# Kernel tuning notes

Hardware: AMD Instinct MI355X
Metric: run time of the kernel (lower is better)

The kernel has to match this reference:

```python
import jax, jax.numpy as jnp
import numpy as np
import math

B, H, N, D = 2, 16, 2048, 128
SM_SCALE = 1.0 / math.sqrt(D)


def setup_inputs() -> dict:
    key = jax.random.key(0)
    kq, kk, kv = jax.random.split(key, 3)
    q = jax.random.normal(kq, (B, H, N, D), dtype=jnp.float32)
    k = jax.random.normal(kk, (B, H, N, D), dtype=jnp.float32)
    v = jax.random.normal(kv, (B, H, N, D), dtype=jnp.float32)
    return {"q": q, "k": k, "v": v}


def reference(q, k, v):
    # RBF-kernel causal attention (non-softmax):
    #   logits_ij = -sm_scale * ||q_i - k_j||^2
    #            = 2*sm_scale*q_i.k_j - sm_scale*||q_i||^2 - sm_scale*||k_j||^2
    #   p = exp(logits) with causal mask (p_ij = 0 for j > i); out = p @ v
    sm_scale = jnp.float32(SM_SCALE)
    q_sq = sm_scale * jnp.sum(q * q, axis=-1)  # [B,H,N]
    k_sq = sm_scale * jnp.sum(k * k, axis=-1)  # [B,H,N]
    qk = jnp.einsum("bhmd,bhnd->bhmn", q, k)
    logits = (2.0 * sm_scale) * qk - q_sq[..., :, None] - k_sq[..., None, :]
    n = q.shape[2]
    causal = jnp.tril(jnp.ones((n, n), dtype=bool))
    logits = jnp.where(causal, logits, -jnp.inf)
    p = jnp.exp(logits)  # NOT normalized (non-softmax attention)
    out = jnp.einsum("bhmn,bhnd->bhmd", p, v)
    return out
```

## Files before the change

kernel.cpp:

```cpp
#include <hip/hip_runtime.h>
#include <math.h>


#define NSEQ 2048
#define DH   128
#define BHC  32
#define SM_SCALE 0.08838834764831845f

typedef __attribute__((ext_vector_type(8))) short    short8;
typedef __attribute__((ext_vector_type(8))) _Float16 half8;
typedef __attribute__((ext_vector_type(4))) short    short4_;
typedef __attribute__((ext_vector_type(4))) float    float4_;
typedef __attribute__((ext_vector_type(4))) unsigned uint4_;
typedef __attribute__((ext_vector_type(2))) unsigned uint2_;

#define KST 136
#define VST 72

__device__ __forceinline__ short f2bf(float x){
  union{float f; unsigned u;} a; a.f=x;
  unsigned r = a.u + 0x7fffu + ((a.u>>16)&1u);
  return (short)(r>>16);
}
__device__ __forceinline__ float bf2f(short h){
  union{float f; unsigned u;} a; a.u=((unsigned)(unsigned short)h)<<16; return a.f;
}
__device__ __forceinline__ unsigned packbf(float a, float b){
  return (unsigned)(unsigned short)f2bf(a) | ((unsigned)(unsigned short)f2bf(b)<<16);
}
__device__ __forceinline__ unsigned cvtpk_bf16(float a, float b){
  unsigned r;
  asm("v_cvt_pk_bf16_f32 %0, %1, %2" : "=v"(r) : "v"(a), "v"(b));
  return r;
}

__device__ __forceinline__ void qswap32(unsigned A, unsigned B, unsigned &X, unsigned &Y){
  uint2_ r = __builtin_amdgcn_permlane32_swap(A, B, false, false);
  X = r[0]; Y = r[1];
}
__device__ __forceinline__ void qswap16(unsigned A, unsigned B, unsigned &X, unsigned &Y, int oddq){
#if __has_builtin(__builtin_amdgcn_permlane16_swap)
  uint2_ r = __builtin_amdgcn_permlane16_swap(A, B, false, false);
  X = r[0]; Y = r[1];
#else
  unsigned As = (unsigned)__builtin_amdgcn_ds_swizzle((int)A, 0x401F);
  unsigned Bs = (unsigned)__builtin_amdgcn_ds_swizzle((int)B, 0x401F);
  X = oddq ? Bs : A;
  Y = oddq ? B  : As;
#endif
}

__global__ __launch_bounds__(256)
void prep_kv5(const float* __restrict__ kg, const float* __restrict__ vg,
              _Float16* __restrict__ khg, short* __restrict__ vtg,
              float* __restrict__ ksqg){
  __shared__ unsigned Vls[128*33];
  const int b = blockIdx.x, t = threadIdx.x;
  const int l = t & 63, wv = t >> 6;
  if(b < 1024){
    const int bh = b>>5, jt = b&31;
    const float4_* vb4 = (const float4_*)(vg + ((size_t)bh*NSEQ + (size_t)jt*64)*DH);
    #pragma unroll
    for(int i=0;i<8;++i){
      float4_ own = vb4[i*256 + t];
      float4_ par;
      par.x = __shfl_xor(own.x, 32); par.y = __shfl_xor(own.y, 32);
      par.z = __shfl_xor(own.z, 32); par.w = __shfl_xor(own.w, 32);
      const int hi = (l>>5)&1;
      unsigned w0 = hi ? packbf(par.z, own.z) : packbf(own.x, par.x);
      unsigned w1 = hi ? packbf(par.w, own.w) : packbf(own.y, par.y);
      const int dd = 4*(t&31) + 2*hi;
      const int j2 = 4*i + wv;
      Vls[dd*33 + j2]     = w0;
      Vls[(dd+1)*33 + j2] = w1;
    }
    __syncthreads();
    short* outp = vtg + ((size_t)(bh*32 + jt)*DH)*64;
    #pragma unroll
    for(int it=0; it<4; ++it){
      int idx = t + 256*it;
      int d = idx>>3, slot = idx&7;
      uint4_ o;
      o.x = Vls[d*33 + 4*slot];   o.y = Vls[d*33 + 4*slot+1];
      o.z = Vls[d*33 + 4*slot+2]; o.w = Vls[d*33 + 4*slot+3];
      *(uint4_*)(outp + d*64 + 8*slot) = o;
    }
  } else {
    const int kb = b - 1024;
    const float4_* kb4 = (const float4_*)(kg + (size_t)kb*64*DH);
    #pragma unroll
    for(int i=0;i<8;++i){
      float4_ x = kb4[i*256 + t];
      const int row = 64*kb + 8*i + (t>>5);
      const int d   = 4*(t&31);
      union{ _Float16 h[4]; uint2_ u; } pk;
      pk.h[0]=(_Float16)x.x; pk.h[1]=(_Float16)x.y;
      pk.h[2]=(_Float16)x.z; pk.h[3]=(_Float16)x.w;
      *(uint2_*)(khg + (size_t)row*DH + d) = pk.u;
      float ss = x.x*x.x + x.y*x.y + x.z*x.z + x.w*x.w;
      ss += __shfl_xor(ss,1);  ss += __shfl_xor(ss,2);
      ss += __shfl_xor(ss,4);  ss += __shfl_xor(ss,8);
      ss += __shfl_xor(ss,16);
      if((l&31)==0) ksqg[row] = SM_SCALE*ss;
    }
  }
}

__global__ __launch_bounds__(256)
void rbf_attn10(const float* __restrict__ qg,
                const _Float16* __restrict__ khg,
                const short* __restrict__ vtg,
                const float* __restrict__ ksqg,
                float* __restrict__ og){
  __shared__ short Kst[2][64*KST];
  __shared__ short Vst[2][128*VST];
  __shared__ float ksLs[2][64];

  const int tid=threadIdx.x;
  const int w=tid>>6, l=tid&63;
  const int quad=l>>4, lr=l&15;
  const int bh=blockIdx.x;
  const int y = blockIdx.y;
  const int t = (y<8) ? y : 23-y;
  const int qbase = 128*t + 32*w;
  const int jtmax = 2*t+1;

  const float*    Qg = qg   + (size_t)bh*NSEQ*DH;
  const _Float16* Kh = khg  + (size_t)bh*NSEQ*DH;
  const short*    Vt = vtg  + (size_t)bh*32*DH*64;
  const float*    Ks = ksqg + (size_t)bh*NSEQ;
  float*          Og = og   + (size_t)bh*NSEQ*DH;

  half8 qf[2][4];
  float qsq[2];
  #pragma unroll
  for(int rt=0;rt<2;++rt){
    const int qrow = qbase + 16*rt + lr;
    const float* qp = Qg + (size_t)qrow*DH + 8*quad;
    float ss=0.f;
    #pragma unroll
    for(int ks=0;ks<4;++ks){
      float4_ a = *(const float4_*)(qp + 32*ks);
      float4_ b = *(const float4_*)(qp + 32*ks + 4);
      half8 h;
      #pragma unroll
      for(int j=0;j<4;++j){
        h[j]   = (_Float16)a[j];
        h[j+4] = (_Float16)b[j];
        ss += a[j]*a[j] + b[j]*b[j];
      }
      qf[rt][ks]=h;
    }
    ss += __shfl_xor(ss,16);
    ss += __shfl_xor(ss,32);
    qsq[rt] = SM_SCALE*ss;
  }

  float4_ oacc[2][8];
  #pragma unroll
  for(int a=0;a<2;++a)
    #pragma unroll
    for(int b2=0;b2<8;++b2) oacc[a][b2] = (float4_)0.f;

  uint4_ kreg[4], vreg[4];
  float  kqreg = 0.f;
  {
    #pragma unroll
    for(int it=0;it<4;++it){
      int idx = tid + 256*it;
      int row = idx>>4, c = idx&15;
      kreg[it] = *(const uint4_*)(Kh + (size_t)row*DH + 8*c);
      int d = idx>>3, slot = idx&7;
      vreg[it] = *(const uint4_*)(Vt + (size_t)d*64 + 8*slot);
    }
    if(tid<64) kqreg = Ks[tid];
  }
  {
    #pragma unroll
    for(int it=0;it<4;++it){
      int idx = tid + 256*it;
      int row = idx>>4, c = idx&15;
      *(uint4_*)&Kst[0][row*KST + 8*c] = kreg[it];
      int d = idx>>3, slot = idx&7;
      *(uint4_*)&Vst[0][d*VST + 8*slot] = vreg[it];
    }
    if(tid<64) ksLs[0][tid] = kqreg;
  }

  int cur = 0;
  for(int jt=0; jt<=jtmax; ++jt){
    __syncthreads();

    if(jt < jtmax){
      const int jc2 = (jt+1)*64;
      #pragma unroll
      for(int it=0;it<4;++it){
        int idx = tid + 256*it;
        int row = idx>>4, c = idx&15;
        kreg[it] = *(const uint4_*)(Kh + (size_t)(jc2+row)*DH + 8*c);
        int d = idx>>3, slot = idx&7;
        vreg[it] = *(const uint4_*)(Vt + ((size_t)(jt+1)*DH + d)*64 + 8*slot);
      }
      if(tid<64) kqreg = Ks[jc2 + tid];
    }

    const int rel = qbase + 31 - 64*jt;
    if(rel >= 0){
      const int ctmax = (rel>>4) < 3 ? (rel>>4) : 3;
      const int nks2  = (rel >= 32) ? 2 : 1;

      float4_ sacc[2][4];
      #pragma unroll
      for(int a=0;a<2;++a)
        #pragma unroll
        for(int ct=0;ct<4;++ct) sacc[a][ct] = (float4_)0.f;

      __builtin_amdgcn_s_setprio(1);
      #pragma unroll
      for(int ks=0;ks<4;++ks){
        half8 kf[4];
        #pragma unroll
        for(int ct=0;ct<4;++ct)
          if(ct<=ctmax) kf[ct] = *(const half8*)&Kst[cur][(16*ct+lr)*KST + 32*ks + 8*quad];
        #pragma unroll
        for(int ct=0;ct<4;++ct)
          if(ct<=ctmax){
            sacc[0][ct]=__builtin_amdgcn_mfma_f32_16x16x32_f16(kf[ct],qf[0][ks],sacc[0][ct],0,0,0);
            sacc[1][ct]=__builtin_amdgcn_mfma_f32_16x16x32_f16(kf[ct],qf[1][ks],sacc[1][ct],0,0,0);
          }
      }
      __builtin_amdgcn_s_setprio(0);

      unsigned pk[2][4][2];
      {
        const int jg0 = 64*jt;
        #pragma unroll
        for(int rt=0;rt<2;++rt){
          const int qrow = qbase + 16*rt + lr;
          const float qs = qsq[rt];
          #pragma unroll
          for(int ct=0;ct<4;++ct){
            if(ct < 2*nks2){
              float4_ kq = *(const float4_*)&ksLs[cur][16*ct + 4*quad];
              const int j0 = jg0 + 16*ct + 4*quad;
              float p[4];
              #pragma unroll
              for(int r=0;r<4;++r){
                float logit = (2.f*SM_SCALE)*sacc[rt][ct][r] - qs - kq[r];
                p[r] = (j0 + r <= qrow) ? __expf(logit) : 0.f;
              }
              pk[rt][ct][0] = cvtpk_bf16(p[0], p[1]);
              pk[rt][ct][1] = cvtpk_bf16(p[2], p[3]);
            }
          }
        }
      }

      __builtin_amdgcn_s_setprio(1);
      #pragma unroll
      for(int ks2=0;ks2<2;++ks2){
        if(ks2 < nks2){
          short8 pf[2];
          #pragma unroll
          for(int rt=0;rt<2;++rt){
            unsigned A0,B0,A1,B1;
            qswap32(pk[rt][2*ks2][0], pk[rt][2*ks2+1][0], A0, B0);
            qswap32(pk[rt][2*ks2][1], pk[rt][2*ks2+1][1], A1, B1);
            unsigned w0,w1,w2,w3;
            qswap16(A0, B0, w0, w2, quad&1);
            qswap16(A1, B1, w1, w3, quad&1);
            union{ uint4_ u; short8 s; } pfu;
            pfu.u.x=w0; pfu.u.y=w1; pfu.u.z=w2; pfu.u.w=w3;
            pf[rt] = pfu.s;
          }
          #pragma unroll
          for(int ctv=0;ctv<8;++ctv){
            const short8 vf = *(const short8*)&Vst[cur][(16*ctv+lr)*VST + 32*ks2 + 8*quad];
            oacc[0][ctv]=__builtin_amdgcn_mfma_f32_16x16x32_bf16(pf[0],vf,oacc[0][ctv],0,0,0);
            oacc[1][ctv]=__builtin_amdgcn_mfma_f32_16x16x32_bf16(pf[1],vf,oacc[1][ctv],0,0,0);
          }
        }
      }
      __builtin_amdgcn_s_setprio(0);
    }

    if(jt < jtmax){
      const int nxt = cur^1;
      #pragma unroll
      for(int it=0;it<4;++it){
        int idx = tid + 256*it;
        int row = idx>>4, c = idx&15;
        *(uint4_*)&Kst[nxt][row*KST + 8*c] = kreg[it];
        int d = idx>>3, slot = idx&7;
        *(uint4_*)&Vst[nxt][d*VST + 8*slot] = vreg[it];
      }
      if(tid<64) ksLs[nxt][tid] = kqreg;
    }
    cur ^= 1;
  }

  #pragma unroll
  for(int rt=0;rt<2;++rt)
    #pragma unroll
    for(int ctv=0;ctv<8;++ctv)
      #pragma unroll
      for(int r=0;r<4;++r){
        const int qrow = qbase + 16*rt + 4*quad + r;
        Og[(size_t)qrow*DH + 16*ctv + lr] = oacc[rt][ctv][r];
      }
}

#define KSTf 136
#define VSTf 36
#define PSTf 72

__global__ __launch_bounds__(256,2)
void rbf_attn_mfma(const float* __restrict__ qg, const float* __restrict__ kg,
                   const float* __restrict__ vg, float* __restrict__ og){
  __shared__ short    Khi[64*KSTf];
  __shared__ short    Klo[64*KSTf];
  __shared__ unsigned VP [128*VSTf];
  __shared__ short    Pfb[64*PSTf];
  __shared__ float    qsq_s[64];
  __shared__ float    ksq_s[64];

  const int tid=threadIdx.x;
  const int w=tid>>6, l=tid&63;
  const int wr=w>>1, wc=w&1;
  const int quad=l>>4, lr=l&15;
  const int bh=blockIdx.x, yp=blockIdx.y;

  const float* Qg = qg + (size_t)bh*NSEQ*DH;
  const float* Kg = kg + (size_t)bh*NSEQ*DH;
  const float* Vg = vg + (size_t)bh*NSEQ*DH;
  float*       Og = og + (size_t)bh*NSEQ*DH;

  for(int pass=0;pass<2;++pass){
    const int m = pass ? (31-yp) : yp;
    __syncthreads();
    short8 qhf[2][4], qlf[2][4];
    #pragma unroll
    for(int rt=0;rt<2;++rt){
      const int grow = m*64 + 32*wr + 16*rt + lr;
      const float* qp = Qg + (size_t)grow*DH + 8*quad;
      float ss=0.f;
      #pragma unroll
      for(int ks=0;ks<4;++ks){
        float4_ a = *(const float4_*)(qp + 32*ks);
        float4_ b = *(const float4_*)(qp + 32*ks + 4);
        short8 hi, lo;
        #pragma unroll
        for(int j=0;j<4;++j){
          float fa=a[j], fb=b[j];
          short ha=f2bf(fa); hi[j]=ha;   lo[j]=f2bf(fa-bf2f(ha));
          short hb=f2bf(fb); hi[j+4]=hb; lo[j+4]=f2bf(fb-bf2f(hb));
          ss += fa*fa + fb*fb;
        }
        qhf[rt][ks]=hi; qlf[rt][ks]=lo;
      }
      ss += __shfl_xor(ss,16);
      ss += __shfl_xor(ss,32);
      if(wc==0 && quad==0) qsq_s[32*wr+16*rt+lr] = SM_SCALE*ss;
    }
    float4_ oacc[2][4];
    #pragma unroll
    for(int a=0;a<2;++a)
      #pragma unroll
      for(int b=0;b<4;++b) oacc[a][b] = (float4_)0.f;

    const int ntiles = m+1;
    for(int jt=0;jt<ntiles;++jt){
      const int jc = jt*64;
      __syncthreads();
      #pragma unroll
      for(int it=0;it<4;++it){
        const int i = tid + 256*it;
        const int row = i>>4, c0 = 8*(i&15);
        const float* kp = Kg + (size_t)(jc+row)*DH + c0;
        float4_ a = *(const float4_*)kp;
        float4_ b = *(const float4_*)(kp+4);
        short8 hi, lo;
        float ss=0.f;
        #pragma unroll
        for(int j=0;j<4;++j){
          float fa=a[j], fb=b[j];
          short ha=f2bf(fa); hi[j]=ha;   lo[j]=f2bf(fa-bf2f(ha));
          short hb=f2bf(fb); hi[j+4]=hb; lo[j+4]=f2bf(fb-bf2f(hb));
          ss += fa*fa + fb*fb;
        }
        ss += __shfl_xor(ss,1); ss += __shfl_xor(ss,2);
        ss += __shfl_xor(ss,4); ss += __shfl_xor(ss,8);
        if(lr==0) ksq_s[row] = SM_SCALE*ss;
        *(short8*)&Khi[row*KSTf + c0] = hi;
        *(short8*)&Klo[row*KSTf + c0] = lo;
      }
      #pragma unroll
      for(int it=0;it<4;++it){
        const int u = tid + 256*it;
        const int d = u & 127, jg = u >> 7;
        const float* vp = Vg + (size_t)(jc + 8*jg)*DH + d;
        float vv[8];
        #pragma unroll
        for(int jj=0;jj<8;++jj) vv[jj] = vp[(size_t)jj*DH];
        uint4_ pk;
        #pragma unroll
        for(int p2=0;p2<4;++p2)
          pk[p2] = (unsigned)(unsigned short)f2bf(vv[2*p2]) |
                   ((unsigned)(unsigned short)f2bf(vv[2*p2+1])<<16);
        *(uint4_*)&VP[d*VSTf + 4*jg] = pk;
      }
      __syncthreads();
      float4_ sacc[2][2];
      #pragma unroll
      for(int a=0;a<2;++a)
        #pragma unroll
        for(int b=0;b<2;++b) sacc[a][b] = (float4_)0.f;
      #pragma unroll
      for(int ks=0;ks<4;++ks){
        short8 khf[2], klf[2];
        #pragma unroll
        for(int ct=0;ct<2;++ct){
          const int off = (32*wc + 16*ct + lr)*KSTf + 32*ks + 8*quad;
          khf[ct] = *(const short8*)&Khi[off];
          klf[ct] = *(const short8*)&Klo[off];
        }
        #pragma unroll
        for(int rt=0;rt<2;++rt)
          #pragma unroll
          for(int ct=0;ct<2;++ct){
            sacc[rt][ct]=__builtin_amdgcn_mfma_f32_16x16x32_bf16(qhf[rt][ks],khf[ct],sacc[rt][ct],0,0,0);
            sacc[rt][ct]=__builtin_amdgcn_mfma_f32_16x16x32_bf16(qhf[rt][ks],klf[ct],sacc[rt][ct],0,0,0);
            sacc[rt][ct]=__builtin_amdgcn_mfma_f32_16x16x32_bf16(qlf[rt][ks],khf[ct],sacc[rt][ct],0,0,0);
          }
      }
      #pragma unroll
      for(int rt=0;rt<2;++rt){
        float qs[4];
        #pragma unroll
        for(int r=0;r<4;++r) qs[r]=qsq_s[32*wr+16*rt+4*quad+r];
        #pragma unroll
        for(int ct=0;ct<2;++ct){
          const float ksq = ksq_s[32*wc+16*ct+lr];
          const int colg = jc + 32*wc+16*ct+lr;
          #pragma unroll
          for(int r=0;r<4;++r){
            const int rowg = m*64 + 32*wr+16*rt+4*quad+r;
            float logit = (2.f*SM_SCALE)*sacc[rt][ct][r] - qs[r] - ksq;
            float p = (colg<=rowg)? __expf(logit) : 0.f;
            Pfb[(32*wr+16*rt+4*quad+r)*PSTf + 32*wc+16*ct+lr] = f2bf(p);
          }
        }
      }
      __syncthreads();
      #pragma unroll
      for(int ks2=0;ks2<2;++ks2){
        short8 pf[2];
        #pragma unroll
        for(int rt=0;rt<2;++rt)
          pf[rt] = *(const short8*)&Pfb[(32*wr+16*rt+lr)*PSTf + 32*ks2 + 8*quad];
        #pragma unroll
        for(int ctv=0;ctv<4;++ctv){
          const int d = 64*wc + 16*ctv + lr;
          const short8 vfb = *(const short8*)((const short*)VP + d*(2*VSTf) + 32*ks2 + 8*quad);
          #pragma unroll
          for(int rt=0;rt<2;++rt)
            oacc[rt][ctv]=__builtin_amdgcn_mfma_f32_16x16x32_bf16(pf[rt],vfb,oacc[rt][ctv],0,0,0);
        }
      }
    }
    #pragma unroll
    for(int rt=0;rt<2;++rt)
      #pragma unroll
      for(int ctv=0;ctv<4;++ctv)
        #pragma unroll
        for(int r=0;r<4;++r){
          const int rowg = m*64 + 32*wr + 16*rt + 4*quad + r;
          Og[(size_t)rowg*DH + 64*wc + 16*ctv + lr] = oacc[rt][ctv][r];
        }
  }
}

extern "C" void kernel_launch(void* const* d_in, const int* in_sizes, int n_in,
                              void* d_out, int out_size, void* d_ws, size_t ws_size,
                              hipStream_t stream) {
  const float* q = (const float*)d_in[0];
  const float* k = (const float*)d_in[1];
  const float* v = (const float*)d_in[2];
  float* out = (float*)d_out;

  const size_t nElem = (size_t)BHC*NSEQ*DH;
  const size_t need  = nElem*2*sizeof(short) + (size_t)BHC*NSEQ*sizeof(float);

  if(ws_size >= need){
    _Float16* khg = (_Float16*)d_ws;
    short*    vtg = (short*)(khg + nElem);
    float*    ksqg = (float*)(vtg + nElem);
    prep_kv5<<<2048, 256, 0, stream>>>(k, v, khg, vtg, ksqg);
    rbf_attn10<<<dim3(BHC,16), 256, 0, stream>>>(q, khg, vtg, ksqg, out);
  } else {
    rbf_attn_mfma<<<dim3(BHC,16), 256, 0, stream>>>(q, k, v, out);
  }
}
```

Measured before the change: 205.0 us.

## Drop LDS staging; each wave streams K/V fragments directly from global memory

The shared-memory double-buffered K/V staging and block-wide barriers are removed. Each wave now owns an independent 32-row query strip, ordered heaviest-first across blocks, and reads K and V MFMA fragments straight from global memory through the cache. A mask-free fast path handles tiles that lie fully below the diagonal. This removes LDS traffic and synchronisation, but waves in a block no longer share loaded tiles, so global and L2 traffic rise and load latency is no longer hidden by a prefetch.

```diff
diff --git a/kernel.cpp b/kernel.cpp
--- a/kernel.cpp
+++ b/kernel.cpp
@@ -13,9 +13,6 @@
 typedef __attribute__((ext_vector_type(4))) float    float4_;
 typedef __attribute__((ext_vector_type(4))) unsigned uint4_;
 typedef __attribute__((ext_vector_type(2))) unsigned uint2_;
-
-#define KST 136
-#define VST 72
 
 __device__ __forceinline__ short f2bf(float x){
   union{float f; unsigned u;} a; a.f=x;
@@ -107,23 +104,18 @@
 }
 
 __global__ __launch_bounds__(256)
-void rbf_attn10(const float* __restrict__ qg,
+void rbf_attn12(const float* __restrict__ qg,
                 const _Float16* __restrict__ khg,
                 const short* __restrict__ vtg,
                 const float* __restrict__ ksqg,
                 float* __restrict__ og){
-  __shared__ short Kst[2][64*KST];
-  __shared__ short Vst[2][128*VST];
-  __shared__ float ksLs[2][64];
-
-  const int tid=threadIdx.x;
-  const int w=tid>>6, l=tid&63;
+  const int tid = threadIdx.x;
+  const int w = tid>>6, l = tid&63;
   const int quad=l>>4, lr=l&15;
-  const int bh=blockIdx.x;
-  const int y = blockIdx.y;
-  const int t = (y<8) ? y : 23-y;
-  const int qbase = 128*t + 32*w;
-  const int jtmax = 2*t+1;
+  const int bh = blockIdx.x;
+  const int y  = blockIdx.y*4 + w;
+  const int qbase = 2016 - 32*y;
+  const int jtmax = (qbase + 31) >> 6;
 
   const float*    Qg = qg   + (size_t)bh*NSEQ*DH;
   const _Float16* Kh = khg  + (size_t)bh*NSEQ*DH;
@@ -162,141 +154,105 @@
     #pragma unroll
     for(int b2=0;b2<8;++b2) oacc[a][b2] = (float4_)0.f;
 
-  uint4_ kreg[4], vreg[4];
-  float  kqreg = 0.f;
-  {
-    #pragma unroll
-    for(int it=0;it<4;++it){
-      int idx = tid + 256*it;
-      int row = idx>>4, c = idx&15;
-      kreg[it] = *(const uint4_*)(Kh + (size_t)row*DH + 8*c);
-      int d = idx>>3, slot = idx&7;
-      vreg[it] = *(const uint4_*)(Vt + (size_t)d*64 + 8*slot);
-    }
-    if(tid<64) kqreg = Ks[tid];
-  }
-  {
-    #pragma unroll
-    for(int it=0;it<4;++it){
-      int idx = tid + 256*it;
-      int row = idx>>4, c = idx&15;
-      *(uint4_*)&Kst[0][row*KST + 8*c] = kreg[it];
-      int d = idx>>3, slot = idx&7;
-      *(uint4_*)&Vst[0][d*VST + 8*slot] = vreg[it];
-    }
-    if(tid<64) ksLs[0][tid] = kqreg;
-  }
-
-  int cur = 0;
+  const _Float16* Kt  = Kh;
+  const short*    Vj  = Vt;
+  const float*    Ksj = Ks;
+
   for(int jt=0; jt<=jtmax; ++jt){
-    __syncthreads();
-
-    if(jt < jtmax){
-      const int jc2 = (jt+1)*64;
-      #pragma unroll
-      for(int it=0;it<4;++it){
-        int idx = tid + 256*it;
-        int row = idx>>4, c = idx&15;
-        kreg[it] = *(const uint4_*)(Kh + (size_t)(jc2+row)*DH + 8*c);
-        int d = idx>>3, slot = idx&7;
-        vreg[it] = *(const uint4_*)(Vt + ((size_t)(jt+1)*DH + d)*64 + 8*slot);
-      }
-      if(tid<64) kqreg = Ks[jc2 + tid];
-    }
-
     const int rel = qbase + 31 - 64*jt;
-    if(rel >= 0){
-      const int ctmax = (rel>>4) < 3 ? (rel>>4) : 3;
-      const int nks2  = (rel >= 32) ? 2 : 1;
-
-      float4_ sacc[2][4];
-      #pragma unroll
-      for(int a=0;a<2;++a)
-        #pragma unroll
-        for(int ct=0;ct<4;++ct) sacc[a][ct] = (float4_)0.f;
-
+    const int ctmax = (rel>>4) < 3 ? (rel>>4) : 3;
+    const int nks2  = (rel >= 32) ? 2 : 1;
+
+    float4_ sacc[2][4];
+    #pragma unroll
+    for(int a=0;a<2;++a)
+      #pragma unroll
+      for(int ct=0;ct<4;++ct) sacc[a][ct] = (float4_)0.f;
+
+    #pragma unroll
+    for(int ks=0;ks<4;++ks){
+      half8 kf[4];
+      #pragma unroll
+      for(int ct=0;ct<4;++ct)
+        if(ct<=ctmax) kf[ct] = *(const half8*)(Kt + (size_t)(16*ct+lr)*DH + 32*ks + 8*quad);
       __builtin_amdgcn_s_setprio(1);
       #pragma unroll
-      for(int ks=0;ks<4;++ks){
-        half8 kf[4];
-        #pragma unroll
-        for(int ct=0;ct<4;++ct)
-          if(ct<=ctmax) kf[ct] = *(const half8*)&Kst[cur][(16*ct+lr)*KST + 32*ks + 8*quad];
-        #pragma unroll
-        for(int ct=0;ct<4;++ct)
-          if(ct<=ctmax){
-            sacc[0][ct]=__builtin_amdgcn_mfma_f32_16x16x32_f16(kf[ct],qf[0][ks],sacc[0][ct],0,0,0);
-            sacc[1][ct]=__builtin_amdgcn_mfma_f32_16x16x32_f16(kf[ct],qf[1][ks],sacc[1][ct],0,0,0);
-          }
-      }
+      for(int ct=0;ct<4;++ct)
+        if(ct<=ctmax){
+          sacc[0][ct]=__builtin_amdgcn_mfma_f32_16x16x32_f16(kf[ct],qf[0][ks],sacc[0][ct],0,0,0);
+          sacc[1][ct]=__builtin_amdgcn_mfma_f32_16x16x32_f16(kf[ct],qf[1][ks],sacc[1][ct],0,0,0);
+        }
       __builtin_amdgcn_s_setprio(0);
-
-      unsigned pk[2][4][2];
-      {
-        const int jg0 = 64*jt;
+    }
+
+    unsigned pk[2][4][2];
+    if(rel >= 94){
+      #pragma unroll
+      for(int ct=0;ct<4;++ct){
+        float4_ kq = *(const float4_*)(Ksj + 16*ct + 4*quad);
         #pragma unroll
         for(int rt=0;rt<2;++rt){
-          const int qrow = qbase + 16*rt + lr;
-          const float qs = qsq[rt];
+          float p[4];
           #pragma unroll
-          for(int ct=0;ct<4;++ct){
-            if(ct < 2*nks2){
-              float4_ kq = *(const float4_*)&ksLs[cur][16*ct + 4*quad];
-              const int j0 = jg0 + 16*ct + 4*quad;
-              float p[4];
-              #pragma unroll
-              for(int r=0;r<4;++r){
-                float logit = (2.f*SM_SCALE)*sacc[rt][ct][r] - qs - kq[r];
-                p[r] = (j0 + r <= qrow) ? __expf(logit) : 0.f;
-              }
-              pk[rt][ct][0] = cvtpk_bf16(p[0], p[1]);
-              pk[rt][ct][1] = cvtpk_bf16(p[2], p[3]);
-            }
-          }
-        }
-      }
-
-      __builtin_amdgcn_s_setprio(1);
-      #pragma unroll
-      for(int ks2=0;ks2<2;++ks2){
-        if(ks2 < nks2){
-          short8 pf[2];
+          for(int r=0;r<4;++r)
+            p[r] = __expf((2.f*SM_SCALE)*sacc[rt][ct][r] - qsq[rt] - kq[r]);
+          pk[rt][ct][0] = cvtpk_bf16(p[0], p[1]);
+          pk[rt][ct][1] = cvtpk_bf16(p[2], p[3]);
+        }
+      }
+    } else {
+      const int jg0 = 64*jt;
+      #pragma unroll
+      for(int ct=0;ct<4;++ct){
+        if(ct < 2*nks2){
+          float4_ kq = *(const float4_*)(Ksj + 16*ct + 4*quad);
+          const int j0 = jg0 + 16*ct + 4*quad;
           #pragma unroll
           for(int rt=0;rt<2;++rt){
-            unsigned A0,B0,A1,B1;
-            qswap32(pk[rt][2*ks2][0], pk[rt][2*ks2+1][0], A0, B0);
-            qswap32(pk[rt][2*ks2][1], pk[rt][2*ks2+1][1], A1, B1);
-            unsigned w0,w1,w2,w3;
-            qswap16(A0, B0, w0, w2, quad&1);
-            qswap16(A1, B1, w1, w3, quad&1);
-            union{ uint4_ u; short8 s; } pfu;
-            pfu.u.x=w0; pfu.u.y=w1; pfu.u.z=w2; pfu.u.w=w3;
-            pf[rt] = pfu.s;
+            const int qrow = qbase + 16*rt + lr;
+            float p[4];
+            #pragma unroll
+            for(int r=0;r<4;++r){
+              float logit = (2.f*SM_SCALE)*sacc[rt][ct][r] - qsq[rt] - kq[r];
+              p[r] = (j0 + r <= qrow) ? __expf(logit) : 0.f;
+            }
+            pk[rt][ct][0] = cvtpk_bf16(p[0], p[1]);
+            pk[rt][ct][1] = cvtpk_bf16(p[2], p[3]);
           }
-          #pragma unroll
-          for(int ctv=0;ctv<8;++ctv){
-            const short8 vf = *(const short8*)&Vst[cur][(16*ctv+lr)*VST + 32*ks2 + 8*quad];
-            oacc[0][ctv]=__builtin_amdgcn_mfma_f32_16x16x32_bf16(pf[0],vf,oacc[0][ctv],0,0,0);
-            oacc[1][ctv]=__builtin_amdgcn_mfma_f32_16x16x32_bf16(pf[1],vf,oacc[1][ctv],0,0,0);
-          }
-        }
-      }
-      __builtin_amdgcn_s_setprio(0);
-    }
-
-    if(jt < jtmax){
-      const int nxt = cur^1;
-      #pragma unroll
-      for(int it=0;it<4;++it){
-        int idx = tid + 256*it;
-        int row = idx>>4, c = idx&15;
-        *(uint4_*)&Kst[nxt][row*KST + 8*c] = kreg[it];
-        int d = idx>>3, slot = idx&7;
-        *(uint4_*)&Vst[nxt][d*VST + 8*slot] = vreg[it];
-      }
-      if(tid<64) ksLs[nxt][tid] = kqreg;
-    }
-    cur ^= 1;
+        }
+      }
+    }
+
+    #pragma unroll
+    for(int ks2=0;ks2<2;++ks2){
+      if(ks2 < nks2){
+        short8 pf[2];
+        #pragma unroll
+        for(int rt=0;rt<2;++rt){
+          unsigned A0,B0,A1,B1;
+          qswap32(pk[rt][2*ks2][0], pk[rt][2*ks2+1][0], A0, B0);
+          qswap32(pk[rt][2*ks2][1], pk[rt][2*ks2+1][1], A1, B1);
+          unsigned w0,w1,w2,w3;
+          qswap16(A0, B0, w0, w2, quad&1);
+          qswap16(A1, B1, w1, w3, quad&1);
+          union{ uint4_ u; short8 s; } pfu;
+          pfu.u.x=w0; pfu.u.y=w1; pfu.u.z=w2; pfu.u.w=w3;
+          pf[rt] = pfu.s;
+        }
+        #pragma unroll
+        for(int ctv=0;ctv<8;++ctv){
+          const short8 vf = *(const short8*)(Vj + (size_t)(16*ctv+lr)*64 + 32*ks2 + 8*quad);
+          __builtin_amdgcn_s_setprio(1);
+          oacc[0][ctv]=__builtin_amdgcn_mfma_f32_16x16x32_bf16(pf[0],vf,oacc[0][ctv],0,0,0);
+          oacc[1][ctv]=__builtin_amdgcn_mfma_f32_16x16x32_bf16(pf[1],vf,oacc[1][ctv],0,0,0);
+          __builtin_amdgcn_s_setprio(0);
+        }
+      }
+    }
+
+    Kt  += 64*DH;
+    Vj  += DH*64;
+    Ksj += 64;
   }
 
   #pragma unroll
@@ -496,7 +452,7 @@
     short*    vtg = (short*)(khg + nElem);
     float*    ksqg = (float*)(vtg + nElem);
     prep_kv5<<<2048, 256, 0, stream>>>(k, v, khg, vtg, ksqg);
-    rbf_attn10<<<dim3(BHC,16), 256, 0, stream>>>(q, khg, vtg, ksqg, out);
+    rbf_attn12<<<dim3(BHC,16), 256, 0, stream>>>(q, khg, vtg, ksqg, out);
   } else {
     rbf_attn_mfma<<<dim3(BHC,16), 256, 0, stream>>>(q, k, v, out);
   }
```

After: 314.6 us. 1.54x slower.
